# Performance work log

Measured on AMD Instinct MI355X. Metric: run time of the kernel, lower is better.

The kernel has to match this reference:

```python
import jax, jax.numpy as jnp
from jax import lax
import numpy as np

DIM = 1024
SEQ = 2048
BATCH = 2
DEPTH = 2
D_INNER = 2 * DIM          # expand=2
D_STATE = 16
D_CONV = 4
DT_RANK = DIM // 16        # ceil(dim/16) = 64
FF = 4 * DIM               # ff_mult=4
EPS = 1e-5


def rmsnorm(x, w, eps=EPS):
    return x * lax.rsqrt(jnp.mean(x * x, axis=-1, keepdims=True) + eps) * w


def layernorm(x, w, b, eps=EPS):
    mu = jnp.mean(x, axis=-1, keepdims=True)
    var = jnp.mean((x - mu) ** 2, axis=-1, keepdims=True)
    return (x - mu) * lax.rsqrt(var + eps) * w + b


def silu(x):
    return x * jax.nn.sigmoid(x)


def causal_conv1d(x, w, b):
    # x: [b, l, d], depthwise causal conv, kernel w: [d, k], bias b: [d]
    xc = jnp.transpose(x, (0, 2, 1))  # [b, d, l]
    y = lax.conv_general_dilated(
        xc, w[:, None, :], window_strides=(1,), padding=[(D_CONV - 1, 0)],
        dimension_numbers=("NCH", "OIH", "NCH"), feature_group_count=D_INNER)
    y = y + b[None, :, None]
    return jnp.transpose(y, (0, 2, 1))  # [b, l, d]


def selective_scan(u, delta, A, B, C, D):
    # u, delta: [b, l, d]; A: [d, n]; B, C: [b, l, n]; D: [d]
    def step(h, inp):
        d_t, b_t, c_t, u_t = inp                       # [b,d],[b,n],[b,n],[b,d]
        dA = jnp.exp(d_t[..., None] * A)               # [b, d, n]
        h = dA * h + (d_t * u_t)[..., None] * b_t[:, None, :]
        y = jnp.einsum("bdn,bn->bd", h, c_t)
        return h, y

    h0 = jnp.zeros((u.shape[0], A.shape[0], A.shape[1]), u.dtype)
    xs = (jnp.swapaxes(delta, 0, 1), jnp.swapaxes(B, 0, 1),
          jnp.swapaxes(C, 0, 1), jnp.swapaxes(u, 0, 1))
    _, ys = lax.scan(step, h0, xs)                     # ys: [l, b, d]
    return jnp.swapaxes(ys, 0, 1) + u * D


def mamba_mixer(h, in_w, cw, cb, xp_w, dtp_w, dtp_b, A_log, D, out_w):
    # h: [b, l, dim]
    xz = jnp.einsum("bld,ed->ble", h, in_w)            # [b, l, 2*d_inner]
    x_in, z = jnp.split(xz, 2, axis=-1)
    x_c = silu(causal_conv1d(x_in, cw, cb))            # [b, l, d_inner]
    x_dbl = jnp.einsum("ble,re->blr", x_c, xp_w)       # [b, l, dt_rank+2n]
    dt = x_dbl[..., :DT_RANK]
    B = x_dbl[..., DT_RANK:DT_RANK + D_STATE]
    C = x_dbl[..., DT_RANK + D_STATE:]
    delta = jax.nn.softplus(jnp.einsum("blr,er->ble", dt, dtp_w) + dtp_b)
    A = -jnp.exp(A_log)
    y = selective_scan(x_c, delta, A, B, C, D)
    y = y * silu(z)
    return jnp.einsum("ble,de->bld", y, out_w)         # [b, l, dim]


def setup_inputs() -> dict:
    key = jax.random.key(0)
    ks = jax.random.split(key, 16)

    def nrm(k, shape, s=0.02):
        return jax.random.normal(k, shape, dtype=jnp.float32) * s

    A_init = jnp.log(jnp.tile(jnp.arange(1, D_STATE + 1, dtype=jnp.float32),
                              (DEPTH, D_INNER, 1)))
    return {
        "x": jax.random.normal(ks[0], (BATCH, SEQ, DIM), jnp.float32),
        "in_proj_w": nrm(ks[1], (DEPTH, 2 * D_INNER, DIM)),
        "conv_w": nrm(ks[2], (DEPTH, D_INNER, D_CONV), 0.1),
        "conv_b": jnp.zeros((DEPTH, D_INNER), jnp.float32),
        "x_proj_w": nrm(ks[3], (DEPTH, DT_RANK + 2 * D_STATE, D_INNER)),
        "dt_proj_w": nrm(ks[4], (DEPTH, D_INNER, DT_RANK), 0.1),
        "dt_proj_b": nrm(ks[5], (DEPTH, D_INNER), 0.1),
        "A_log": A_init,
        "D": jnp.ones((DEPTH, D_INNER), jnp.float32),
        "out_proj_w": nrm(ks[6], (DEPTH, DIM, D_INNER)),
        "rms_w": jnp.ones((DEPTH, DIM), jnp.float32),
        "ln_w": jnp.ones((DEPTH, DIM), jnp.float32),
        "ln_b": jnp.zeros((DEPTH, DIM), jnp.float32),
        "ff_w1": nrm(ks[7], (2 * FF, DIM)),
        "ff_b1": jnp.zeros((2 * FF,), jnp.float32),
        "ff_w2": nrm(ks[8], (DIM, FF)),
        "ff_b2": jnp.zeros((DIM,), jnp.float32),
    }


def reference(x, in_proj_w, conv_w, conv_b, x_proj_w, dt_proj_w, dt_proj_b,
              A_log, D, out_proj_w, rms_w, ln_w, ln_b, ff_w1, ff_b1, ff_w2, ff_b2):
    residual = None
    h = x
    for i in range(in_proj_w.shape[0]):
        # fused add + RMSNorm (prenorm, residual in fp32)
        residual = h if residual is None else residual + h
        normed = rmsnorm(residual, rms_w[i])
        h = mamba_mixer(normed, in_proj_w[i], conv_w[i], conv_b[i],
                        x_proj_w[i], dt_proj_w[i], dt_proj_b[i],
                        A_log[i], D[i], out_proj_w[i])
        # extra per-block LayerNorm on mixer output
        h = layernorm(h, ln_w[i], ln_b[i])
    # final GEGLU feedforward
    u = jnp.einsum("bld,ed->ble", h, ff_w1) + ff_b1    # [b, l, 2*FF]
    a, g = jnp.split(u, 2, axis=-1)
    v = a * jax.nn.gelu(g, approximate=False)
    return jnp.einsum("blf,df->bld", v, ff_w2) + ff_b2
```

## Files before the change

### kernel.cpp

```cpp
#include <hip/hip_runtime.h>
#include <cstdint>
#include <cstddef>

#define DIM     1024
#define SEQ     2048
#define BATCH   2
#define DEPTH   2
#define D_INNER 2048
#define D_STATE 16
#define D_CONV  4
#define DT_RANK 64
#define FF      4096
#define ROWS    (BATCH*SEQ)
#define EPS     1e-5f

#define CS      32
#define NC      (SEQ/CS)
#define NC_LOG  6

#define XP_KS    8
#define XP_KSTEP (D_INNER/XP_KS)

#define LOG2E 1.44269504088896f

typedef unsigned short ushort_t;
typedef short bf16x8 __attribute__((ext_vector_type(8)));
typedef float f32x4  __attribute__((ext_vector_type(4)));

__device__ __forceinline__ float sigmoidf_(float x) { return 1.f / (1.f + __expf(-x)); }

__device__ __forceinline__ ushort_t f2bf(float x) {
  unsigned int u = __float_as_uint(x);
  u += 0x7fffu + ((u >> 16) & 1u);
  return (ushort_t)(u >> 16);
}
__device__ __forceinline__ float bf2f(ushort_t u) {
  return __uint_as_float((unsigned)u << 16);
}

__device__ __forceinline__ void async_cp16(const void* g, void* lds) {
  __builtin_amdgcn_global_load_lds(
      (const __attribute__((address_space(1))) unsigned int*)g,
      (__attribute__((address_space(3))) unsigned int*)lds, 16, 0, 0);
}

__device__ __forceinline__ float2 block_sum2(float a, float b) {
#pragma unroll
  for (int off = 32; off > 0; off >>= 1) {
    a += __shfl_down(a, off, 64);
    b += __shfl_down(b, off, 64);
  }
  __shared__ float sa[4], sb[4];
  __syncthreads();
  if ((threadIdx.x & 63) == 0) { int w = threadIdx.x >> 6; sa[w] = a; sb[w] = b; }
  __syncthreads();
  return make_float2(sa[0] + sa[1] + sa[2] + sa[3], sb[0] + sb[1] + sb[2] + sb[3]);
}

__global__ __launch_bounds__(256) void res_rms_kernel(
    const float* __restrict__ xin,
    float* __restrict__ res, ushort_t* __restrict__ nrm, const float* __restrict__ w) {
  int row = blockIdx.x;
  const float* xr = xin + (size_t)row * DIM;
  float* rr = res + (size_t)row * DIM;
  ushort_t* nr = nrm + (size_t)row * DIM;
  float v[4]; float ss = 0.f;
#pragma unroll
  for (int i = 0; i < 4; ++i) {
    int j = threadIdx.x + i * 256;
    float t = xr[j];
    v[i] = t; rr[j] = t; ss += t * t;
  }
  float2 s = block_sum2(ss, 0.f);
  float rstd = rsqrtf(s.x * (1.f / DIM) + EPS);
#pragma unroll
  for (int i = 0; i < 4; ++i) {
    int j = threadIdx.x + i * 256;
    nr[j] = f2bf(v[i] * rstd * w[j]);
  }
}

__global__ __launch_bounds__(256) void ln_res_rms_kernel(
    const float* __restrict__ in, float* __restrict__ res,
    const float* __restrict__ lw, const float* __restrict__ lb,
    const float* __restrict__ rw, ushort_t* __restrict__ nrm) {
  int row = blockIdx.x;
  const float* xr = in + (size_t)row * DIM;
  float* rr = res + (size_t)row * DIM;
  ushort_t* nr = nrm + (size_t)row * DIM;
  float v[4]; float s1 = 0.f, s2 = 0.f;
#pragma unroll
  for (int i = 0; i < 4; ++i) {
    int j = threadIdx.x + i * 256;
    float t = xr[j];
    v[i] = t; s1 += t; s2 += t * t;
  }
  float2 s = block_sum2(s1, s2);
  float mean = s.x * (1.f / DIM);
  float var = s.y * (1.f / DIM) - mean * mean;
  float rstd = rsqrtf(var + EPS);
  float t4[4]; float ss = 0.f;
#pragma unroll
  for (int i = 0; i < 4; ++i) {
    int j = threadIdx.x + i * 256;
    float o = (v[i] - mean) * rstd * lw[j] + lb[j];
    float t = rr[j] + o;
    rr[j] = t;
    t4[i] = t; ss += t * t;
  }
  float2 s2v = block_sum2(ss, 0.f);
  float rstd2 = rsqrtf(s2v.x * (1.f / DIM) + EPS);
#pragma unroll
  for (int i = 0; i < 4; ++i) {
    int j = threadIdx.x + i * 256;
    nr[j] = f2bf(t4[i] * rstd2 * rw[j]);
  }
}

__global__ __launch_bounds__(256) void ln_final_kernel(
    const float* __restrict__ in, ushort_t* __restrict__ outb,
    const float* __restrict__ w, const float* __restrict__ b) {
  int row = blockIdx.x;
  const float* xr = in + (size_t)row * DIM;
  ushort_t* obrow = outb + (size_t)row * DIM;
  float v[4]; float s1 = 0.f, s2 = 0.f;
#pragma unroll
  for (int i = 0; i < 4; ++i) {
    int j = threadIdx.x + i * 256;
    float t = xr[j];
    v[i] = t; s1 += t; s2 += t * t;
  }
  float2 s = block_sum2(s1, s2);
  float mean = s.x * (1.f / DIM);
  float var = s.y * (1.f / DIM) - mean * mean;
  float rstd = rsqrtf(var + EPS);
#pragma unroll
  for (int i = 0; i < 4; ++i) {
    int j = threadIdx.x + i * 256;
    obrow[j] = f2bf((v[i] - mean) * rstd * w[j] + b[j]);
  }
}

__global__ __launch_bounds__(256) void f2b_all(
    const float* __restrict__ w0, ushort_t* __restrict__ d0,
    const float* __restrict__ w1, ushort_t* __restrict__ d1,
    const float* __restrict__ w2, ushort_t* __restrict__ d2,
    const float* __restrict__ w3, ushort_t* __restrict__ d3) {
  int i = (blockIdx.x * 256 + threadIdx.x) * 4;
  const float* s; ushort_t* d; int off;
  if (i < 8388608)        { s = w0; d = d0; off = i; }
  else if (i < 12582912)  { s = w1; d = d1; off = i - 8388608; }
  else if (i < 20971520)  { s = w2; d = d2; off = i - 12582912; }
  else                    { s = w3; d = d3; off = i - 20971520; }
  float4 v = *reinterpret_cast<const float4*>(s + off);
  d[off + 0] = f2bf(v.x); d[off + 1] = f2bf(v.y);
  d[off + 2] = f2bf(v.z); d[off + 3] = f2bf(v.w);
}

__global__ __launch_bounds__(256) void gemm_bf16_nt(
    const ushort_t* __restrict__ A,
    const ushort_t* __restrict__ B,
    float* __restrict__ C,
    ushort_t* __restrict__ Cb,
    int N, int K,
    const float* __restrict__ bias, int grp) {
  __shared__ ushort_t As[128 * 64];
  __shared__ ushort_t Bs[128 * 64];
  const int tid = threadIdx.x;
  const int l = tid & 63;
  const int w = tid >> 6;

  const unsigned nwgx = gridDim.x;
  const unsigned nwg = nwgx * gridDim.y;
  const unsigned bid = blockIdx.y * nwgx + blockIdx.x;
  const unsigned cpx = nwg >> 3;
  const unsigned s = (bid & 7u) * cpx + (bid >> 3);
  const unsigned bandw = (unsigned)grp * nwgx;
  const unsigned band = s / bandw;
  const unsigned rem = s % bandw;
  const int m0 = (int)(band * grp + (rem % grp)) * 128;
  const int n0 = (int)(rem / grp) * 128;

  const int wm = (w >> 1) * 64;
  const int wn = (w & 1) * 64;

  const int srow = l >> 3;
  const int ksrc = 8 * ((l & 7) ^ srow);
  const int kg = l >> 4;
  const int lr = l & 15;

  f32x4 acc[4][4];
#pragma unroll
  for (int mi = 0; mi < 4; ++mi)
#pragma unroll
    for (int ni = 0; ni < 4; ++ni) acc[mi][ni] = (f32x4)0.f;

  for (int k0 = 0; k0 < K; k0 += 64) {
#pragma unroll
    for (int j = 0; j < 4; ++j) {
      int c = j * 4 + w;
      int r = c * 8 + srow;
      async_cp16(&A[(size_t)(m0 + r) * K + k0 + ksrc], &As[c * 512]);
    }
#pragma unroll
    for (int j = 0; j < 4; ++j) {
      int c = j * 4 + w;
      int r = c * 8 + srow;
      async_cp16(&B[(size_t)(n0 + r) * K + k0 + ksrc], &Bs[c * 512]);
    }
    __syncthreads();
#pragma unroll
    for (int ks = 0; ks < 2; ++ks) {
      bf16x8 af[4], bfr[4];
#pragma unroll
      for (int mi = 0; mi < 4; ++mi) {
        int r = wm + mi * 16 + lr;
        int boff = r * 128 + ((ks * 64 + kg * 16) ^ ((r & 7) << 4));
        af[mi] = *reinterpret_cast<const bf16x8*>(reinterpret_cast<const char*>(As) + boff);
      }
#pragma unroll
      for (int ni = 0; ni < 4; ++ni) {
        int r = wn + ni * 16 + lr;
        int boff = r * 128 + ((ks * 64 + kg * 16) ^ ((r & 7) << 4));
        bfr[ni] = *reinterpret_cast<const bf16x8*>(reinterpret_cast<const char*>(Bs) + boff);
      }
#pragma unroll
      for (int mi = 0; mi < 4; ++mi)
#pragma unroll
        for (int ni = 0; ni < 4; ++ni)
          acc[mi][ni] = __builtin_amdgcn_mfma_f32_16x16x32_bf16(af[mi], bfr[ni], acc[mi][ni], 0, 0, 0);
    }
    __syncthreads();
  }

  const int crow0 = (l >> 4) * 4;
  const int ccol = l & 15;
#pragma unroll
  for (int mi = 0; mi < 4; ++mi) {
#pragma unroll
    for (int ni = 0; ni < 4; ++ni) {
      int col = n0 + wn + ni * 16 + ccol;
      float bv = bias ? bias[col] : 0.f;
#pragma unroll
      for (int j = 0; j < 4; ++j) {
        int row = m0 + wm + mi * 16 + crow0 + j;
        float v = acc[mi][ni][j] + bv;
        if (Cb) Cb[(size_t)row * N + col] = f2bf(v);
        else    C[(size_t)row * N + col] = v;
      }
    }
  }
}

__global__ __launch_bounds__(256) void gemm_bf16_nt64(
    const ushort_t* __restrict__ A,
    const ushort_t* __restrict__ B,
    float* __restrict__ C,
    int N, int K,
    const float* __restrict__ bias, int grp) {
  __shared__ ushort_t As[64 * 64];
  __shared__ ushort_t Bs[128 * 64];
  const int tid = threadIdx.x;
  const int l = tid & 63;
  const int w = tid >> 6;

  const unsigned nwgx = gridDim.x;
  const unsigned nwg = nwgx * gridDim.y;
  const unsigned bid = blockIdx.y * nwgx + blockIdx.x;
  const unsigned cpx = nwg >> 3;
  const unsigned s = (bid & 7u) * cpx + (bid >> 3);
  const unsigned bandw = (unsigned)grp * nwgx;
  const unsigned band = s / bandw;
  const unsigned rem = s % bandw;
  const int m0 = (int)(band * grp + (rem % grp)) * 64;
  const int n0 = (int)(rem / grp) * 128;

  const int wm = (w >> 1) * 32;
  const int wn = (w & 1) * 64;

  const int srow = l >> 3;
  const int ksrc = 8 * ((l & 7) ^ srow);
  const int kg = l >> 4;
  const int lr = l & 15;

  f32x4 acc[2][4];
#pragma unroll
  for (int mi = 0; mi < 2; ++mi)
#pragma unroll
    for (int ni = 0; ni < 4; ++ni) acc[mi][ni] = (f32x4)0.f;

  for (int k0 = 0; k0 < K; k0 += 64) {
#pragma unroll
    for (int j = 0; j < 2; ++j) {
      int c = j * 4 + w;
      int r = c * 8 + srow;
      async_cp16(&A[(size_t)(m0 + r) * K + k0 + ksrc], &As[c * 512]);
    }
#pragma unroll
    for (int j = 0; j < 4; ++j) {
      int c = j * 4 + w;
      int r = c * 8 + srow;
      async_cp16(&B[(size_t)(n0 + r) * K + k0 + ksrc], &Bs[c * 512]);
    }
    __syncthreads();
#pragma unroll
    for (int ks = 0; ks < 2; ++ks) {
      bf16x8 af[2], bfr[4];
#pragma unroll
      for (int mi = 0; mi < 2; ++mi) {
        int r = wm + mi * 16 + lr;
        int boff = r * 128 + ((ks * 64 + kg * 16) ^ ((r & 7) << 4));
        af[mi] = *reinterpret_cast<const bf16x8*>(reinterpret_cast<const char*>(As) + boff);
      }
#pragma unroll
      for (int ni = 0; ni < 4; ++ni) {
        int r = wn + ni * 16 + lr;
        int boff = r * 128 + ((ks * 64 + kg * 16) ^ ((r & 7) << 4));
        bfr[ni] = *reinterpret_cast<const bf16x8*>(reinterpret_cast<const char*>(Bs) + boff);
      }
#pragma unroll
      for (int mi = 0; mi < 2; ++mi)
#pragma unroll
        for (int ni = 0; ni < 4; ++ni)
          acc[mi][ni] = __builtin_amdgcn_mfma_f32_16x16x32_bf16(af[mi], bfr[ni], acc[mi][ni], 0, 0, 0);
    }
    __syncthreads();
  }

  const int crow0 = (l >> 4) * 4;
  const int ccol = l & 15;
#pragma unroll
  for (int mi = 0; mi < 2; ++mi) {
#pragma unroll
    for (int ni = 0; ni < 4; ++ni) {
      int col = n0 + wn + ni * 16 + ccol;
      float bv = bias ? bias[col] : 0.f;
#pragma unroll
      for (int j = 0; j < 4; ++j) {
        int row = m0 + wm + mi * 16 + crow0 + j;
        C[(size_t)row * N + col] = acc[mi][ni][j] + bv;
      }
    }
  }
}

__global__ __launch_bounds__(256) void gemm_ffn1_glu(
    const ushort_t* __restrict__ A,
    const ushort_t* __restrict__ B,
    ushort_t* __restrict__ O,
    int K,
    const float* __restrict__ bias, int grp) {
  __shared__ ushort_t As[128 * 64];
  __shared__ ushort_t Bs[128 * 64];
  const int tid = threadIdx.x;
  const int l = tid & 63;
  const int w = tid >> 6;

  const unsigned nwgx = gridDim.x;
  const unsigned nwg = nwgx * gridDim.y;
  const unsigned bid = blockIdx.y * nwgx + blockIdx.x;
  const unsigned cpx = nwg >> 3;
  const unsigned s = (bid & 7u) * cpx + (bid >> 3);
  const unsigned bandw = (unsigned)grp * nwgx;
  const unsigned band = s / bandw;
  const unsigned rem = s % bandw;
  const int m0 = (int)(band * grp + (rem % grp)) * 128;
  const int n0 = (int)(rem / grp) * 64;

  const int wm = (w >> 1) * 64;
  const int wn2 = (w & 1) * 32;

  const int srow = l >> 3;
  const int ksrc = 8 * ((l & 7) ^ srow);
  const int kg = l >> 4;
  const int lr = l & 15;

  f32x4 acc[4][4];
#pragma unroll
  for (int mi = 0; mi < 4; ++mi)
#pragma unroll
    for (int ni = 0; ni < 4; ++ni) acc[mi][ni] = (f32x4)0.f;

  for (int k0 = 0; k0 < K; k0 += 64) {
#pragma unroll
    for (int j = 0; j < 4; ++j) {
      int c = j * 4 + w;
      int r = c * 8 + srow;
      async_cp16(&A[(size_t)(m0 + r) * K + k0 + ksrc], &As[c * 512]);
    }
#pragma unroll
    for (int j = 0; j < 4; ++j) {
      int c = j * 4 + w;
      int gr = (c < 8) ? (n0 + c * 8 + srow)
                       : (FF + n0 + (c - 8) * 8 + srow);
      async_cp16(&B[(size_t)gr * K + k0 + ksrc], &Bs[c * 512]);
    }
    __syncthreads();
#pragma unroll
    for (int ks = 0; ks < 2; ++ks) {
      bf16x8 af[4], bfr[4];
#pragma unroll
      for (int mi = 0; mi < 4; ++mi) {
        int r = wm + mi * 16 + lr;
        int boff = r * 128 + ((ks * 64 + kg * 16) ^ ((r & 7) << 4));
        af[mi] = *reinterpret_cast<const bf16x8*>(reinterpret_cast<const char*>(As) + boff);
      }
#pragma unroll
      for (int ni = 0; ni < 4; ++ni) {
        int r = (ni < 2 ? wn2 + ni * 16 : 64 + wn2 + (ni - 2) * 16) + lr;
        int boff = r * 128 + ((ks * 64 + kg * 16) ^ ((r & 7) << 4));
        bfr[ni] = *reinterpret_cast<const bf16x8*>(reinterpret_cast<const char*>(Bs) + boff);
      }
#pragma unroll
      for (int mi = 0; mi < 4; ++mi)
#pragma unroll
        for (int ni = 0; ni < 4; ++ni)
          acc[mi][ni] = __builtin_amdgcn_mfma_f32_16x16x32_bf16(af[mi], bfr[ni], acc[mi][ni], 0, 0, 0);
    }
    __syncthreads();
  }

  const int crow0 = (l >> 4) * 4;
  const int ccol = l & 15;
#pragma unroll
  for (int mi = 0; mi < 4; ++mi) {
#pragma unroll
    for (int ni = 0; ni < 2; ++ni) {
      int col = n0 + wn2 + ni * 16 + ccol;
      float ba = bias[col];
      float bg = bias[FF + col];
#pragma unroll
      for (int j = 0; j < 4; ++j) {
        int row = m0 + wm + mi * 16 + crow0 + j;
        float a = acc[mi][ni][j] + ba;
        float g = acc[mi][ni + 2][j] + bg;
        float ge = 0.5f * g * (1.f + erff(g * 0.70710678118654752f));
        O[(size_t)row * FF + col] = f2bf(a * ge);
      }
    }
  }
}

__global__ __launch_bounds__(256) void gemm_nt(
    const float* __restrict__ A, int lda,
    const float* __restrict__ B, int ldb,
    float* __restrict__ C, int ldc,
    int N, int K,
    const float* __restrict__ bias, int act) {
  __shared__ __align__(16) float Asf[16][68];
  __shared__ __align__(16) float Bsf[16][68];
  const int tx = threadIdx.x;
  const int ty = threadIdx.y;
  const int tid = ty * 16 + tx;
  const int m0 = blockIdx.y * 64;
  const int n0 = blockIdx.x * 64;
  const int lrow = tid >> 2;
  const int lk = (tid & 3) * 4;

  float acc[4][4] = {{0.f}};

  for (int k0 = 0; k0 < K; k0 += 16) {
    float4 av, bv;
    {
      const float* ap = A + (size_t)(m0 + lrow) * lda + k0 + lk;
      av = *reinterpret_cast<const float4*>(ap);
    }
    int brow = n0 + lrow;
    if (brow < N) {
      const float* bp = B + (size_t)brow * ldb + k0 + lk;
      bv = *reinterpret_cast<const float4*>(bp);
    } else {
      bv = make_float4(0.f, 0.f, 0.f, 0.f);
    }
    __syncthreads();
    Asf[lk + 0][lrow] = av.x; Asf[lk + 1][lrow] = av.y;
    Asf[lk + 2][lrow] = av.z; Asf[lk + 3][lrow] = av.w;
    Bsf[lk + 0][lrow] = bv.x; Bsf[lk + 1][lrow] = bv.y;
    Bsf[lk + 2][lrow] = bv.z; Bsf[lk + 3][lrow] = bv.w;
    __syncthreads();
#pragma unroll
    for (int k = 0; k < 16; ++k) {
      const float4 a4 = *reinterpret_cast<const float4*>(&Asf[k][ty * 4]);
      const float4 b4 = *reinterpret_cast<const float4*>(&Bsf[k][tx * 4]);
      float a[4] = {a4.x, a4.y, a4.z, a4.w};
      float bb[4] = {b4.x, b4.y, b4.z, b4.w};
#pragma unroll
      for (int i = 0; i < 4; ++i)
#pragma unroll
        for (int j = 0; j < 4; ++j)
          acc[i][j] = fmaf(a[i], bb[j], acc[i][j]);
    }
  }

#pragma unroll
  for (int i = 0; i < 4; ++i) {
    int m = m0 + ty * 4 + i;
#pragma unroll
    for (int j = 0; j < 4; ++j) {
      int n = n0 + tx * 4 + j;
      if (n < N) {
        float v = acc[i][j];
        if (bias) v += bias[n];
        if (act == 1) v = (v > 20.f) ? v : log1pf(__expf(v));
        C[(size_t)m * ldc + n] = v;
      }
    }
  }
}

__global__ __launch_bounds__(256) void xproj_partial(
    const ushort_t* __restrict__ A,
    const float* __restrict__ W,
    float* __restrict__ pbuf) {
  __shared__ __align__(16) float As[64][68];
  __shared__ __align__(16) float Wsd[96][68];
  const int ks = blockIdx.x;
  const int mb = blockIdx.y;
  const int tid = threadIdx.x;
  const int r0 = (tid >> 4) * 4;
  const int c0 = (tid & 15) * 6;

  float acc[4][6];
#pragma unroll
  for (int i = 0; i < 4; ++i)
#pragma unroll
    for (int j = 0; j < 6; ++j) acc[i][j] = 0.f;

  for (int k0 = 0; k0 < XP_KSTEP; k0 += 64) {
    const int kbase = ks * XP_KSTEP + k0;
    __syncthreads();
    {
      int r = tid >> 2, c = (tid & 3) * 16;
      const ushort_t* src = A + (size_t)(mb * 64 + r) * D_INNER + kbase + c;
#pragma unroll
      for (int q = 0; q < 4; ++q) {
        ushort4 uv = *reinterpret_cast<const ushort4*>(src + q * 4);
        As[r][c + q * 4 + 0] = bf2f(uv.x);
        As[r][c + q * 4 + 1] = bf2f(uv.y);
        As[r][c + q * 4 + 2] = bf2f(uv.z);
        As[r][c + q * 4 + 3] = bf2f(uv.w);
      }
    }
#pragma unroll
    for (int q = 0; q < 6; ++q) {
      int f = q * 256 + tid;
      int wr = f >> 4;
      int wc = (f & 15) * 4;
      *reinterpret_cast<float4*>(&Wsd[wr][wc]) =
          *reinterpret_cast<const float4*>(&W[(size_t)wr * D_INNER + kbase + wc]);
    }
    __syncthreads();
#pragma unroll 16
    for (int k = 0; k < 64; ++k) {
      float a[4], wv[6];
#pragma unroll
      for (int i = 0; i < 4; ++i) a[i] = As[r0 + i][k];
#pragma unroll
      for (int j = 0; j < 6; ++j) wv[j] = Wsd[c0 + j][k];
#pragma unroll
      for (int i = 0; i < 4; ++i)
#pragma unroll
        for (int j = 0; j < 6; ++j)
          acc[i][j] = fmaf(a[i], wv[j], acc[i][j]);
    }
  }

  float* dst = pbuf + ((size_t)ks * ROWS + mb * 64) * 96;
#pragma unroll
  for (int i = 0; i < 4; ++i)
#pragma unroll
    for (int j = 0; j < 6; ++j)
      dst[(size_t)(r0 + i) * 96 + c0 + j] = acc[i][j];
}

__global__ __launch_bounds__(256) void xproj_reduce(
    const float* __restrict__ pbuf, float* __restrict__ xdbl) {
  int i = blockIdx.x * 256 + threadIdx.x;
  float s = 0.f;
#pragma unroll
  for (int ks = 0; ks < XP_KS; ++ks)
    s += pbuf[(size_t)ks * (ROWS * 96) + i];
  xdbl[i] = s;
}

__global__ __launch_bounds__(256) void conv_silu_kernel(
    const ushort_t* __restrict__ xzb, ushort_t* __restrict__ xcb,
    const float* __restrict__ cw, const float* __restrict__ cb) {
  int t = (blockIdx.x * 256 + threadIdx.x) * 4;
  if (t >= ROWS * D_INNER) return;
  int d = t & (D_INNER - 1);
  int row = t >> 11;
  int l = row & (SEQ - 1);
  float acc[4];
#pragma unroll
  for (int q = 0; q < 4; ++q) acc[q] = cb[d + q];
#pragma unroll
  for (int j = 0; j < 4; ++j) {
    int ls = l - 3 + j;
    if (ls >= 0) {
      ushort4 uv = *reinterpret_cast<const ushort4*>(
          xzb + (size_t)(row - 3 + j) * (2 * D_INNER) + d);
      acc[0] = fmaf(cw[(d + 0) * 4 + j], bf2f(uv.x), acc[0]);
      acc[1] = fmaf(cw[(d + 1) * 4 + j], bf2f(uv.y), acc[1]);
      acc[2] = fmaf(cw[(d + 2) * 4 + j], bf2f(uv.z), acc[2]);
      acc[3] = fmaf(cw[(d + 3) * 4 + j], bf2f(uv.w), acc[3]);
    }
  }
  ushort4 o;
  o.x = f2bf(acc[0] * sigmoidf_(acc[0]));
  o.y = f2bf(acc[1] * sigmoidf_(acc[1]));
  o.z = f2bf(acc[2] * sigmoidf_(acc[2]));
  o.w = f2bf(acc[3] * sigmoidf_(acc[3]));
  *reinterpret_cast<ushort4*>(xcb + t) = o;
}

__global__ __launch_bounds__(256) void scan_pass1(
    const float* __restrict__ delta,
    const ushort_t* __restrict__ xcb,
    const float* __restrict__ xdbl,
    const float* __restrict__ A_log,
    float* __restrict__ harr,
    float* __restrict__ dtsum) {
  __shared__ __align__(16) float Bls[CS][16];
  int gid = blockIdx.x * 256 + threadIdx.x;
  int d = gid & (D_INNER - 1);
  int bc = gid >> 11;
  int c = bc & (NC - 1);
  int b = bc >> NC_LOG;
  const size_t r0 = (size_t)b * SEQ + (size_t)c * CS;

  if (threadIdx.x < CS * 4) {
    int sl = threadIdx.x >> 2, sf = (threadIdx.x & 3) * 4;
    *reinterpret_cast<f32x4*>(&Bls[sl][sf]) =
        *reinterpret_cast<const f32x4*>(xdbl + (r0 + sl) * 96 + 64 + sf);
  }

  float Av2[D_STATE];
#pragma unroll
  for (int n = 0; n < D_STATE; ++n)
    Av2[n] = -__expf(A_log[(size_t)d * D_STATE + n]) * LOG2E;
  float h[D_STATE];
#pragma unroll
  for (int n = 0; n < D_STATE; ++n) h[n] = 0.f;
  float dts = 0.f;

  const float* drow = delta + r0 * D_INNER + d;
  const ushort_t* urow = xcb + r0 * D_INNER + d;

  float pdt[4], pu[4];
#pragma unroll
  for (int g = 0; g < 4; ++g) {
    pdt[g] = drow[(size_t)g * D_INNER];
    pu[g]  = bf2f(urow[(size_t)g * D_INNER]);
  }
  __syncthreads();

  for (int l0 = 0; l0 < CS; l0 += 4) {
    float cdt[4], cu[4];
#pragma unroll
    for (int g = 0; g < 4; ++g) { cdt[g] = pdt[g]; cu[g] = pu[g]; }
    if (l0 + 4 < CS) {
#pragma unroll
      for (int g = 0; g < 4; ++g) {
        pdt[g] = drow[(size_t)(l0 + 4 + g) * D_INNER];
        pu[g]  = bf2f(urow[(size_t)(l0 + 4 + g) * D_INNER]);
      }
    }
#pragma unroll
    for (int g = 0; g < 4; ++g) {
      int l = l0 + g;
      f32x4 B0 = *reinterpret_cast<const f32x4*>(&Bls[l][0]);
      f32x4 B1 = *reinterpret_cast<const f32x4*>(&Bls[l][4]);
      f32x4 B2 = *reinterpret_cast<const f32x4*>(&Bls[l][8]);
      f32x4 B3 = *reinterpret_cast<const f32x4*>(&Bls[l][12]);
      float du = cdt[g] * cu[g];
      dts += cdt[g];
      float Bsr[D_STATE] = {B0[0],B0[1],B0[2],B0[3], B1[0],B1[1],B1[2],B1[3],
                            B2[0],B2[1],B2[2],B2[3], B3[0],B3[1],B3[2],B3[3]};
#pragma unroll
      for (int n = 0; n < D_STATE; ++n) {
        float dA = __builtin_amdgcn_exp2f(cdt[g] * Av2[n]);
        h[n] = dA * h[n] + du * Bsr[n];
      }
    }
  }
#pragma unroll
  for (int n = 0; n < D_STATE; ++n)
    harr[((size_t)bc * D_STATE + n) * D_INNER + d] = h[n];
  dtsum[(size_t)bc * D_INNER + d] = dts;
}

__global__ __launch_bounds__(256) void scan_pass2(
    float* __restrict__ harr,
    const float* __restrict__ dtsum,
    const float* __restrict__ A_log) {
  int gid = blockIdx.x * 256 + threadIdx.x;
  int d = gid & (D_INNER - 1);
  int bn = gid >> 11;
  int n = bn & (D_STATE - 1);
  int b = bn >> 4;
  float Av2 = -__expf(A_log[(size_t)d * D_STATE + n]) * LOG2E;
  float h = 0.f;
  for (int c = 0; c < NC; ++c) {
    size_t bc = (size_t)b * NC + c;
    size_t idx = (bc * D_STATE + n) * D_INNER + d;
    float he = harr[idx];
    harr[idx] = h;
    float P = __builtin_amdgcn_exp2f(Av2 * dtsum[bc * D_INNER + d]);
    h = P * h + he;
  }
}

__global__ __launch_bounds__(256) void scan_pass3(
    const float* __restrict__ delta,
    const ushort_t* __restrict__ xcb,
    ushort_t* __restrict__ ybf,
    const float* __restrict__ xdbl,
    const ushort_t* __restrict__ xzb,
    const float* __restrict__ A_log,
    const float* __restrict__ Dp,
    const float* __restrict__ harr) {
  __shared__ __align__(16) float BCls[CS][32];
  int gid = blockIdx.x * 256 + threadIdx.x;
  int d = gid & (D_INNER - 1);
  int bc = gid >> 11;
  int c = bc & (NC - 1);
  int b = bc >> NC_LOG;
  const size_t r0 = (size_t)b * SEQ + (size_t)c * CS;

  {
    int sl = threadIdx.x >> 3, sf = (threadIdx.x & 7) * 4;
    *reinterpret_cast<f32x4*>(&BCls[sl][sf]) =
        *reinterpret_cast<const f32x4*>(xdbl + (r0 + sl) * 96 + 64 + sf);
  }

  float Av2[D_STATE];
#pragma unroll
  for (int n = 0; n < D_STATE; ++n)
    Av2[n] = -__expf(A_log[(size_t)d * D_STATE + n]) * LOG2E;
  const float Dd = Dp[d];
  float h[D_STATE];
#pragma unroll
  for (int n = 0; n < D_STATE; ++n)
    h[n] = harr[((size_t)bc * D_STATE + n) * D_INNER + d];

  const float* drow = delta + r0 * D_INNER + d;
  const ushort_t* urow = xcb + r0 * D_INNER + d;
  const ushort_t* zrow = xzb + r0 * (2 * D_INNER) + D_INNER + d;
  ushort_t* yrow = ybf + r0 * D_INNER + d;

  float pdt[4], pu[4], pz[4];
#pragma unroll
  for (int g = 0; g < 4; ++g) {
    pdt[g] = drow[(size_t)g * D_INNER];
    pu[g]  = bf2f(urow[(size_t)g * D_INNER]);
    pz[g]  = bf2f(zrow[(size_t)g * (2 * D_INNER)]);
  }
  __syncthreads();

  for (int l0 = 0; l0 < CS; l0 += 4) {
    float cdt[4], cu[4], cz[4];
#pragma unroll
    for (int g = 0; g < 4; ++g) { cdt[g] = pdt[g]; cu[g] = pu[g]; cz[g] = pz[g]; }
    if (l0 + 4 < CS) {
#pragma unroll
      for (int g = 0; g < 4; ++g) {
        pdt[g] = drow[(size_t)(l0 + 4 + g) * D_INNER];
        pu[g]  = bf2f(urow[(size_t)(l0 + 4 + g) * D_INNER]);
        pz[g]  = bf2f(zrow[(size_t)(l0 + 4 + g) * (2 * D_INNER)]);
      }
    }
#pragma unroll
    for (int g = 0; g < 4; ++g) {
      int l = l0 + g;
      f32x4 B0 = *reinterpret_cast<const f32x4*>(&BCls[l][0]);
      f32x4 B1 = *reinterpret_cast<const f32x4*>(&BCls[l][4]);
      f32x4 B2 = *reinterpret_cast<const f32x4*>(&BCls[l][8]);
      f32x4 B3 = *reinterpret_cast<const f32x4*>(&BCls[l][12]);
      f32x4 C0 = *reinterpret_cast<const f32x4*>(&BCls[l][16]);
      f32x4 C1 = *reinterpret_cast<const f32x4*>(&BCls[l][20]);
      f32x4 C2 = *reinterpret_cast<const f32x4*>(&BCls[l][24]);
      f32x4 C3 = *reinterpret_cast<const f32x4*>(&BCls[l][28]);
      float du = cdt[g] * cu[g];
      float Bsr[D_STATE] = {B0[0],B0[1],B0[2],B0[3], B1[0],B1[1],B1[2],B1[3],
                            B2[0],B2[1],B2[2],B2[3], B3[0],B3[1],B3[2],B3[3]};
      float Csr[D_STATE] = {C0[0],C0[1],C0[2],C0[3], C1[0],C1[1],C1[2],C1[3],
                            C2[0],C2[1],C2[2],C2[3], C3[0],C3[1],C3[2],C3[3]};
      float y = 0.f;
#pragma unroll
      for (int n = 0; n < D_STATE; ++n) {
        float dA = __builtin_amdgcn_exp2f(cdt[g] * Av2[n]);
        h[n] = dA * h[n] + du * Bsr[n];
        y = fmaf(h[n], Csr[n], y);
      }
      y = fmaf(cu[g], Dd, y);
      yrow[(size_t)l * D_INNER] = f2bf(y * (cz[g] * sigmoidf_(cz[g])));
    }
  }
}

extern "C" void kernel_launch(void* const* d_in, const int* in_sizes, int n_in,
                              void* d_out, int out_size, void* d_ws, size_t ws_size,
                              hipStream_t stream) {
  const float* x         = (const float*)d_in[0];
  const float* in_proj_w = (const float*)d_in[1];
  const float* conv_w    = (const float*)d_in[2];
  const float* conv_b    = (const float*)d_in[3];
  const float* x_proj_w  = (const float*)d_in[4];
  const float* dt_proj_w = (const float*)d_in[5];
  const float* dt_proj_b = (const float*)d_in[6];
  const float* A_log     = (const float*)d_in[7];
  const float* Dp        = (const float*)d_in[8];
  const float* out_proj_w= (const float*)d_in[9];
  const float* rms_w     = (const float*)d_in[10];
  const float* ln_w      = (const float*)d_in[11];
  const float* ln_b      = (const float*)d_in[12];
  const float* ff_w1     = (const float*)d_in[13];
  const float* ff_b1     = (const float*)d_in[14];
  const float* ff_w2     = (const float*)d_in[15];
  const float* ff_b2     = (const float*)d_in[16];
  float* out = (float*)d_out;

  float* ws = (float*)d_ws;
  float* res     = ws;
  float* dtsum   = ws + 4194304;
  float* xdbl    = ws + 8388608;
  ushort_t* hbuf_bf = (ushort_t*)(ws + 8912896);
  float*    pbuf    = ws + 11010048;
  ushort_t* y_bf    = (ushort_t*)(ws + 15204352);
  ushort_t* glu_bf  = (ushort_t*)(ws + 11010048);
  float* big   = ws + 19398656;
  ushort_t* xz_bf = (ushort_t*)big;
  ushort_t* xcb   = (ushort_t*)(big + 8388608);
  float* delta = big + 16777216;
  float* harr  = big + 25165824;
  float* op_out= big;
  ushort_t* nrm_bf = (ushort_t*)delta;
  ushort_t* in_w_bf  = (ushort_t*)(ws + 52953088);
  ushort_t* out_w_bf = (ushort_t*)(ws + 57147392);
  ushort_t* ff1_bf   = (ushort_t*)(ws + 59244544);
  ushort_t* ff2_bf   = (ushort_t*)(ws + 63438848);

  dim3 tb(16, 16);

  f2b_all<<<24576, 256, 0, stream>>>(in_proj_w, in_w_bf, out_proj_w, out_w_bf,
                                     ff_w1, ff1_bf, ff_w2, ff2_bf);

  res_rms_kernel<<<ROWS, 256, 0, stream>>>(x, res, nrm_bf, rms_w);

  for (int i = 0; i < DEPTH; ++i) {
    const float* cw    = conv_w + (size_t)i * D_INNER * D_CONV;
    const float* cb    = conv_b + (size_t)i * D_INNER;
    const float* xp_w  = x_proj_w + (size_t)i * 96 * D_INNER;
    const float* dtp_w = dt_proj_w + (size_t)i * D_INNER * DT_RANK;
    const float* dtp_b = dt_proj_b + (size_t)i * D_INNER;
    const float* Alg   = A_log + (size_t)i * D_INNER * D_STATE;
    const float* Di    = Dp + (size_t)i * D_INNER;

    gemm_bf16_nt<<<dim3(32, 32), 256, 0, stream>>>(
        nrm_bf, in_w_bf + (size_t)i * 4194304, nullptr, xz_bf, 2 * D_INNER, DIM,
        nullptr, 16);
    conv_silu_kernel<<<(ROWS * D_INNER / 4) / 256, 256, 0, stream>>>(xz_bf, xcb, cw, cb);
    xproj_partial<<<dim3(XP_KS, 64), 256, 0, stream>>>(xcb, xp_w, pbuf);
    xproj_reduce<<<(ROWS * 96) / 256, 256, 0, stream>>>(pbuf, xdbl);
    gemm_nt<<<dim3(32, 64), tb, 0, stream>>>(xdbl, 96, dtp_w, DT_RANK, delta, D_INNER,
                                             D_INNER, DT_RANK, dtp_b, 1);
    scan_pass1<<<(BATCH * NC * D_INNER) / 256, 256, 0, stream>>>(delta, xcb, xdbl, Alg,
                                                                 harr, dtsum);
    scan_pass2<<<(BATCH * D_STATE * D_INNER) / 256, 256, 0, stream>>>(harr, dtsum, Alg);
    scan_pass3<<<(BATCH * NC * D_INNER) / 256, 256, 0, stream>>>(delta, xcb, y_bf, xdbl,
                                                                 xz_bf, Alg, Di, harr);
    gemm_bf16_nt64<<<dim3(8, 64), 256, 0, stream>>>(
        y_bf, out_w_bf + (size_t)i * 2097152, op_out, DIM, D_INNER, nullptr, 8);
    if (i + 1 < DEPTH) {
      ln_res_rms_kernel<<<ROWS, 256, 0, stream>>>(
          op_out, res, ln_w + (size_t)i * DIM, ln_b + (size_t)i * DIM,
          rms_w + (size_t)(i + 1) * DIM, nrm_bf);
    } else {
      ln_final_kernel<<<ROWS, 256, 0, stream>>>(
          op_out, hbuf_bf, ln_w + (size_t)i * DIM, ln_b + (size_t)i * DIM);
    }
  }

  gemm_ffn1_glu<<<dim3(64, 32), 256, 0, stream>>>(hbuf_bf, ff1_bf, glu_bf, DIM,
                                                  ff_b1, 16);
  gemm_bf16_nt64<<<dim3(8, 64), 256, 0, stream>>>(glu_bf, ff2_bf, out, DIM, FF,
                                                  ff_b2, 8);
}
```

Before: 759.9 us.

## Double-buffer LDS tiles in bf16 GEMM and GEGLU FFN kernels

Converts the NT bf16 GEMM and the fused FFN1 GEGLU GEMM main loops to a two-stage LDS ping-pong. The async global-to-LDS copies for the next K tile are issued before computing on the current tile, with vmcnt waits and raw barriers in place of __syncthreads. This is meant to hide global load latency behind MFMA work. In exchange it doubles LDS use to 64 KB per block, which can cut occupancy, and it relies on a hand-counted vmcnt value staying correct.

```diff
diff --git a/kernel.cpp b/kernel.cpp
--- a/kernel.cpp
+++ b/kernel.cpp
@@ -164,8 +164,8 @@
     ushort_t* __restrict__ Cb,
     int N, int K,
     const float* __restrict__ bias, int grp) {
-  __shared__ ushort_t As[128 * 64];
-  __shared__ ushort_t Bs[128 * 64];
+  __shared__ ushort_t As[2][128 * 64];
+  __shared__ ushort_t Bs[2][128 * 64];
   const int tid = threadIdx.x;
   const int l = tid & 63;
   const int w = tid >> 6;
@@ -195,43 +195,69 @@
 #pragma unroll
     for (int ni = 0; ni < 4; ++ni) acc[mi][ni] = (f32x4)0.f;
 
-  for (int k0 = 0; k0 < K; k0 += 64) {
-#pragma unroll
-    for (int j = 0; j < 4; ++j) {
-      int c = j * 4 + w;
-      int r = c * 8 + srow;
-      async_cp16(&A[(size_t)(m0 + r) * K + k0 + ksrc], &As[c * 512]);
-    }
-#pragma unroll
-    for (int j = 0; j < 4; ++j) {
-      int c = j * 4 + w;
-      int r = c * 8 + srow;
-      async_cp16(&B[(size_t)(n0 + r) * K + k0 + ksrc], &Bs[c * 512]);
-    }
-    __syncthreads();
-#pragma unroll
-    for (int ks = 0; ks < 2; ++ks) {
-      bf16x8 af[4], bfr[4];
-#pragma unroll
-      for (int mi = 0; mi < 4; ++mi) {
-        int r = wm + mi * 16 + lr;
-        int boff = r * 128 + ((ks * 64 + kg * 16) ^ ((r & 7) << 4));
-        af[mi] = *reinterpret_cast<const bf16x8*>(reinterpret_cast<const char*>(As) + boff);
-      }
-#pragma unroll
-      for (int ni = 0; ni < 4; ++ni) {
-        int r = wn + ni * 16 + lr;
-        int boff = r * 128 + ((ks * 64 + kg * 16) ^ ((r & 7) << 4));
-        bfr[ni] = *reinterpret_cast<const bf16x8*>(reinterpret_cast<const char*>(Bs) + boff);
-      }
-#pragma unroll
-      for (int mi = 0; mi < 4; ++mi)
-#pragma unroll
-        for (int ni = 0; ni < 4; ++ni)
-          acc[mi][ni] = __builtin_amdgcn_mfma_f32_16x16x32_bf16(af[mi], bfr[ni], acc[mi][ni], 0, 0, 0);
-    }
-    __syncthreads();
-  }
+  const int nt = K >> 6;
+
+#define STAGE_NT(buf, t)                                                      \
+  do {                                                                        \
+    int k0_ = (t) << 6;                                                       \
+    _Pragma("unroll")                                                         \
+    for (int j = 0; j < 4; ++j) {                                             \
+      int c = j * 4 + w;                                                      \
+      int r = c * 8 + srow;                                                   \
+      async_cp16(&A[(size_t)(m0 + r) * K + k0_ + ksrc], &As[buf][c * 512]);   \
+    }                                                                         \
+    _Pragma("unroll")                                                         \
+    for (int j = 0; j < 4; ++j) {                                             \
+      int c = j * 4 + w;                                                      \
+      int r = c * 8 + srow;                                                   \
+      async_cp16(&B[(size_t)(n0 + r) * K + k0_ + ksrc], &Bs[buf][c * 512]);   \
+    }                                                                         \
+  } while (0)
+
+#define COMPUTE_NT(buf)                                                       \
+  do {                                                                        \
+    _Pragma("unroll")                                                         \
+    for (int ks = 0; ks < 2; ++ks) {                                          \
+      bf16x8 af[4], bfr[4];                                                   \
+      _Pragma("unroll")                                                       \
+      for (int mi = 0; mi < 4; ++mi) {                                        \
+        int r = wm + mi * 16 + lr;                                            \
+        int boff = r * 128 + ((ks * 64 + kg * 16) ^ ((r & 7) << 4));          \
+        af[mi] = *reinterpret_cast<const bf16x8*>(                            \
+            reinterpret_cast<const char*>(As[buf]) + boff);                   \
+      }                                                                       \
+      _Pragma("unroll")                                                       \
+      for (int ni = 0; ni < 4; ++ni) {                                        \
+        int r = wn + ni * 16 + lr;                                            \
+        int boff = r * 128 + ((ks * 64 + kg * 16) ^ ((r & 7) << 4));          \
+        bfr[ni] = *reinterpret_cast<const bf16x8*>(                           \
+            reinterpret_cast<const char*>(Bs[buf]) + boff);                   \
+      }                                                                       \
+      _Pragma("unroll")                                                       \
+      for (int mi = 0; mi < 4; ++mi)                                          \
+        _Pragma("unroll")                                                     \
+        for (int ni = 0; ni < 4; ++ni)                                        \
+          acc[mi][ni] = __builtin_amdgcn_mfma_f32_16x16x32_bf16(              \
+              af[mi], bfr[ni], acc[mi][ni], 0, 0, 0);                         \
+    }                                                                         \
+  } while (0)
+
+  STAGE_NT(0, 0);
+  int cur = 0;
+  for (int t = 0; t < nt; ++t) {
+    if (t + 1 < nt) {
+      STAGE_NT(cur ^ 1, t + 1);
+      asm volatile("s_waitcnt vmcnt(8)" ::: "memory");
+    } else {
+      asm volatile("s_waitcnt vmcnt(0)" ::: "memory");
+    }
+    asm volatile("s_barrier" ::: "memory");
+    COMPUTE_NT(cur);
+    asm volatile("s_barrier" ::: "memory");
+    cur ^= 1;
+  }
+#undef STAGE_NT
+#undef COMPUTE_NT
 
   const int crow0 = (l >> 4) * 4;
   const int ccol = l & 15;
@@ -350,8 +376,8 @@
     ushort_t* __restrict__ O,
     int K,
     const float* __restrict__ bias, int grp) {
-  __shared__ ushort_t As[128 * 64];
-  __shared__ ushort_t Bs[128 * 64];
+  __shared__ ushort_t As[2][128 * 64];
+  __shared__ ushort_t Bs[2][128 * 64];
   const int tid = threadIdx.x;
   const int l = tid & 63;
   const int w = tid >> 6;
@@ -381,44 +407,70 @@
 #pragma unroll
     for (int ni = 0; ni < 4; ++ni) acc[mi][ni] = (f32x4)0.f;
 
-  for (int k0 = 0; k0 < K; k0 += 64) {
-#pragma unroll
-    for (int j = 0; j < 4; ++j) {
-      int c = j * 4 + w;
-      int r = c * 8 + srow;
-      async_cp16(&A[(size_t)(m0 + r) * K + k0 + ksrc], &As[c * 512]);
-    }
-#pragma unroll
-    for (int j = 0; j < 4; ++j) {
-      int c = j * 4 + w;
-      int gr = (c < 8) ? (n0 + c * 8 + srow)
-                       : (FF + n0 + (c - 8) * 8 + srow);
-      async_cp16(&B[(size_t)gr * K + k0 + ksrc], &Bs[c * 512]);
-    }
-    __syncthreads();
-#pragma unroll
-    for (int ks = 0; ks < 2; ++ks) {
-      bf16x8 af[4], bfr[4];
-#pragma unroll
-      for (int mi = 0; mi < 4; ++mi) {
-        int r = wm + mi * 16 + lr;
-        int boff = r * 128 + ((ks * 64 + kg * 16) ^ ((r & 7) << 4));
-        af[mi] = *reinterpret_cast<const bf16x8*>(reinterpret_cast<const char*>(As) + boff);
-      }
-#pragma unroll
-      for (int ni = 0; ni < 4; ++ni) {
-        int r = (ni < 2 ? wn2 + ni * 16 : 64 + wn2 + (ni - 2) * 16) + lr;
-        int boff = r * 128 + ((ks * 64 + kg * 16) ^ ((r & 7) << 4));
-        bfr[ni] = *reinterpret_cast<const bf16x8*>(reinterpret_cast<const char*>(Bs) + boff);
-      }
-#pragma unroll
-      for (int mi = 0; mi < 4; ++mi)
-#pragma unroll
-        for (int ni = 0; ni < 4; ++ni)
-          acc[mi][ni] = __builtin_amdgcn_mfma_f32_16x16x32_bf16(af[mi], bfr[ni], acc[mi][ni], 0, 0, 0);
-    }
-    __syncthreads();
-  }
+  const int nt = K >> 6;
+
+#define STAGE_FG(buf, t)                                                      \
+  do {                                                                        \
+    int k0_ = (t) << 6;                                                       \
+    _Pragma("unroll")                                                         \
+    for (int j = 0; j < 4; ++j) {                                             \
+      int c = j * 4 + w;                                                      \
+      int r = c * 8 + srow;                                                   \
+      async_cp16(&A[(size_t)(m0 + r) * K + k0_ + ksrc], &As[buf][c * 512]);   \
+    }                                                                         \
+    _Pragma("unroll")                                                         \
+    for (int j = 0; j < 4; ++j) {                                             \
+      int c = j * 4 + w;                                                      \
+      int gr = (c < 8) ? (n0 + c * 8 + srow)                                  \
+                       : (FF + n0 + (c - 8) * 8 + srow);                      \
+      async_cp16(&B[(size_t)gr * K + k0_ + ksrc], &Bs[buf][c * 512]);         \
+    }                                                                         \
+  } while (0)
+
+#define COMPUTE_FG(buf)                                                       \
+  do {                                                                        \
+    _Pragma("unroll")                                                         \
+    for (int ks = 0; ks < 2; ++ks) {                                          \
+      bf16x8 af[4], bfr[4];                                                   \
+      _Pragma("unroll")                                                       \
+      for (int mi = 0; mi < 4; ++mi) {                                        \
+        int r = wm + mi * 16 + lr;                                            \
+        int boff = r * 128 + ((ks * 64 + kg * 16) ^ ((r & 7) << 4));          \
+        af[mi] = *reinterpret_cast<const bf16x8*>(                            \
+            reinterpret_cast<const char*>(As[buf]) + boff);                   \
+      }                                                                       \
+      _Pragma("unroll")                                                       \
+      for (int ni = 0; ni < 4; ++ni) {                                        \
+        int r = (ni < 2 ? wn2 + ni * 16 : 64 + wn2 + (ni - 2) * 16) + lr;     \
+        int boff = r * 128 + ((ks * 64 + kg * 16) ^ ((r & 7) << 4));          \
+        bfr[ni] = *reinterpret_cast<const bf16x8*>(                           \
+            reinterpret_cast<const char*>(Bs[buf]) + boff);                   \
+      }                                                                       \
+      _Pragma("unroll")                                                       \
+      for (int mi = 0; mi < 4; ++mi)                                          \
+        _Pragma("unroll")                                                     \
+        for (int ni = 0; ni < 4; ++ni)                                        \
+          acc[mi][ni] = __builtin_amdgcn_mfma_f32_16x16x32_bf16(              \
+              af[mi], bfr[ni], acc[mi][ni], 0, 0, 0);                         \
+    }                                                                         \
+  } while (0)
+
+  STAGE_FG(0, 0);
+  int cur = 0;
+  for (int t = 0; t < nt; ++t) {
+    if (t + 1 < nt) {
+      STAGE_FG(cur ^ 1, t + 1);
+      asm volatile("s_waitcnt vmcnt(8)" ::: "memory");
+    } else {
+      asm volatile("s_waitcnt vmcnt(0)" ::: "memory");
+    }
+    asm volatile("s_barrier" ::: "memory");
+    COMPUTE_FG(cur);
+    asm volatile("s_barrier" ::: "memory");
+    cur ^= 1;
+  }
+#undef STAGE_FG
+#undef COMPUTE_FG
 
   const int crow0 = (l >> 4) * 4;
   const int ccol = l & 15;
```

New measurement: 756.8 us. No clear change (-0.4%).

## Double-buffer LDS tiles in bf16 NT GEMM to overlap loads with MFMA

Applied to the files above, without the earlier changes.

Doubles the shared-memory A/B tiles in gemm_bf16_nt and prefetches the next K-tile with async copies while the current tile is consumed by MFMA, using explicit vmcnt waits and raw s_barrier instead of __syncthreads. This is meant to hide global-to-LDS latency behind compute. It doubles LDS use to 64KB per block, which can lower occupancy. The hand-written waitcnt/barrier sequencing is fragile if the compiler reorders LDS reads across the asm barriers.

```diff
diff --git a/kernel.cpp b/kernel.cpp
--- a/kernel.cpp
+++ b/kernel.cpp
@@ -164,8 +164,8 @@
     ushort_t* __restrict__ Cb,
     int N, int K,
     const float* __restrict__ bias, int grp) {
-  __shared__ ushort_t As[128 * 64];
-  __shared__ ushort_t Bs[128 * 64];
+  __shared__ ushort_t As[2][128 * 64];
+  __shared__ ushort_t Bs[2][128 * 64];
   const int tid = threadIdx.x;
   const int l = tid & 63;
   const int w = tid >> 6;
@@ -195,43 +195,69 @@
 #pragma unroll
     for (int ni = 0; ni < 4; ++ni) acc[mi][ni] = (f32x4)0.f;
 
-  for (int k0 = 0; k0 < K; k0 += 64) {
-#pragma unroll
-    for (int j = 0; j < 4; ++j) {
-      int c = j * 4 + w;
-      int r = c * 8 + srow;
-      async_cp16(&A[(size_t)(m0 + r) * K + k0 + ksrc], &As[c * 512]);
-    }
-#pragma unroll
-    for (int j = 0; j < 4; ++j) {
-      int c = j * 4 + w;
-      int r = c * 8 + srow;
-      async_cp16(&B[(size_t)(n0 + r) * K + k0 + ksrc], &Bs[c * 512]);
-    }
-    __syncthreads();
-#pragma unroll
-    for (int ks = 0; ks < 2; ++ks) {
-      bf16x8 af[4], bfr[4];
-#pragma unroll
-      for (int mi = 0; mi < 4; ++mi) {
-        int r = wm + mi * 16 + lr;
-        int boff = r * 128 + ((ks * 64 + kg * 16) ^ ((r & 7) << 4));
-        af[mi] = *reinterpret_cast<const bf16x8*>(reinterpret_cast<const char*>(As) + boff);
-      }
-#pragma unroll
-      for (int ni = 0; ni < 4; ++ni) {
-        int r = wn + ni * 16 + lr;
-        int boff = r * 128 + ((ks * 64 + kg * 16) ^ ((r & 7) << 4));
-        bfr[ni] = *reinterpret_cast<const bf16x8*>(reinterpret_cast<const char*>(Bs) + boff);
-      }
-#pragma unroll
-      for (int mi = 0; mi < 4; ++mi)
-#pragma unroll
-        for (int ni = 0; ni < 4; ++ni)
-          acc[mi][ni] = __builtin_amdgcn_mfma_f32_16x16x32_bf16(af[mi], bfr[ni], acc[mi][ni], 0, 0, 0);
-    }
-    __syncthreads();
-  }
+  const int nt = K >> 6;
+
+#define STAGE_NT(buf, t)                                                      \
+  do {                                                                        \
+    int k0_ = (t) << 6;                                                       \
+    _Pragma("unroll")                                                         \
+    for (int j = 0; j < 4; ++j) {                                             \
+      int c = j * 4 + w;                                                      \
+      int r = c * 8 + srow;                                                   \
+      async_cp16(&A[(size_t)(m0 + r) * K + k0_ + ksrc], &As[buf][c * 512]);   \
+    }                                                                         \
+    _Pragma("unroll")                                                         \
+    for (int j = 0; j < 4; ++j) {                                             \
+      int c = j * 4 + w;                                                      \
+      int r = c * 8 + srow;                                                   \
+      async_cp16(&B[(size_t)(n0 + r) * K + k0_ + ksrc], &Bs[buf][c * 512]);   \
+    }                                                                         \
+  } while (0)
+
+#define COMPUTE_NT(buf)                                                       \
+  do {                                                                        \
+    _Pragma("unroll")                                                         \
+    for (int ks = 0; ks < 2; ++ks) {                                          \
+      bf16x8 af[4], bfr[4];                                                   \
+      _Pragma("unroll")                                                       \
+      for (int mi = 0; mi < 4; ++mi) {                                        \
+        int r = wm + mi * 16 + lr;                                            \
+        int boff = r * 128 + ((ks * 64 + kg * 16) ^ ((r & 7) << 4));          \
+        af[mi] = *reinterpret_cast<const bf16x8*>(                            \
+            reinterpret_cast<const char*>(As[buf]) + boff);                   \
+      }                                                                       \
+      _Pragma("unroll")                                                       \
+      for (int ni = 0; ni < 4; ++ni) {                                        \
+        int r = wn + ni * 16 + lr;                                            \
+        int boff = r * 128 + ((ks * 64 + kg * 16) ^ ((r & 7) << 4));          \
+        bfr[ni] = *reinterpret_cast<const bf16x8*>(                           \
+            reinterpret_cast<const char*>(Bs[buf]) + boff);                   \
+      }                                                                       \
+      _Pragma("unroll")                                                       \
+      for (int mi = 0; mi < 4; ++mi)                                          \
+        _Pragma("unroll")                                                     \
+        for (int ni = 0; ni < 4; ++ni)                                        \
+          acc[mi][ni] = __builtin_amdgcn_mfma_f32_16x16x32_bf16(              \
+              af[mi], bfr[ni], acc[mi][ni], 0, 0, 0);                         \
+    }                                                                         \
+  } while (0)
+
+  STAGE_NT(0, 0);
+  int cur = 0;
+  for (int t = 0; t < nt; ++t) {
+    if (t + 1 < nt) {
+      STAGE_NT(cur ^ 1, t + 1);
+      asm volatile("s_waitcnt vmcnt(8)" ::: "memory");
+    } else {
+      asm volatile("s_waitcnt vmcnt(0)" ::: "memory");
+    }
+    asm volatile("s_barrier" ::: "memory");
+    COMPUTE_NT(cur);
+    asm volatile("s_barrier" ::: "memory");
+    cur ^= 1;
+  }
+#undef STAGE_NT
+#undef COMPUTE_NT
 
   const int crow0 = (l >> 4) * 4;
   const int ccol = l & 15;
```

After: 748.1 us. About the same (-1.6%).
